# Performance work log

Measured on AMD Instinct MI355X. Metric: run time of the kernel, lower is better.

Reference implementation:

```python
import jax, jax.numpy as jnp
import numpy as np
import math

B, SQ, SK, H, D = 4, 2048, 2048, 16, 128
IS_CAUSAL = True
SCALE = 1.0 / math.sqrt(D)


def setup_inputs() -> dict:
    key = jax.random.key(0)
    kq, kk, kv = jax.random.split(key, 3)
    query = jax.random.normal(kq, (B, SQ, H, D), dtype=jnp.float32)
    key_t = jax.random.normal(kk, (B, SK, H, D), dtype=jnp.float32)
    value = jax.random.normal(kv, (B, SK, H, D), dtype=jnp.float32)
    return {"query": query, "key": key_t, "value": value}


def reference(query, key, value):
    # q: [B, Sq, H, D], k: [B, Sk, H, D], v: [B, Sk, H, Dv]
    scores = jnp.einsum('bqhd,bkhd->bhqk', query, key) * SCALE  # [B, H, Sq, Sk]
    if IS_CAUSAL:
        causal = jnp.triu(jnp.ones((SQ, SK), dtype=jnp.bool_), k=1)  # True above diag
        scores = jnp.where(causal[None, None, :, :], jnp.float32(-jnp.inf), scores)
    attn = jax.nn.softmax(scores, axis=-1)  # stable softmax (== exp(scores - lse))
    out = jnp.einsum('bhqk,bkhd->bqhd', attn, value)  # [B, Sq, H, Dv]
    return out
```

## Files before the change

### kernel.cpp

```cpp
#include <hip/hip_runtime.h>
#include <hip/hip_bf16.h>

typedef float  f32x16 __attribute__((ext_vector_type(16)));
typedef float  f32x4  __attribute__((ext_vector_type(4)));
typedef short  s16x8  __attribute__((ext_vector_type(8)));
typedef unsigned int u32x4 __attribute__((ext_vector_type(4)));

#define B_   4
#define SQ_  2048
#define SK_  2048
#define H_   16
#define D_   128
#define RS   (H_*D_)
#define QSCALE 0.12751219658526f
#define KVB  64
#define QTILE 256
#define KB_BYTES  (64*128*2)
#define BUF_BYTES (2*KB_BYTES)

__device__ __forceinline__ unsigned pk_bf16(float lo, float hi) {
    unsigned r;
    asm("v_cvt_pk_bf16_f32 %0, %1, %2" : "=v"(r) : "v"(lo), "v"(hi));
    return r;
}
__device__ __forceinline__ void swap32u(unsigned &a, unsigned &b) {
    asm("v_permlane32_swap_b32 %0, %1" : "+v"(a), "+v"(b));
}
__device__ __forceinline__ int kaddr(int row, int colb) {
    return row * 256 + (colb ^ ((row & 7) << 4));
}
__device__ __forceinline__ int vaddr(int d, int colb) {
    return d * 128 + (colb ^ ((((d & 7) ^ ((d >> 3) & 7))) << 4));
}

__global__ __launch_bounds__(512, 2)
void fattn_fwd(const float* __restrict__ Qg, const float* __restrict__ Kg,
               const float* __restrict__ Vg, float* __restrict__ Og)
{
    __shared__ __align__(16) char smem[2 * BUF_BYTES];

    const int tid = threadIdx.x;
    const int w   = tid >> 6;
    const int l   = tid & 63;
    const int l31 = l & 31;
    const int hi  = l >> 5;

    const int i    = blockIdx.x;
    const int orig = (i & 7) * 64 + (i >> 3);
    const int bh   = orig >> 3;
    const int j    = orig & 7;
    const int tile = ((bh >> 2) & 1) ? j : 7 - j;
    const int b    = bh >> 4;
    const int h    = bh & 15;

    const int q0 = tile * QTILE;
    const int nt = (q0 + QTILE) / KVB;

    const size_t base = ((size_t)b * SK_ * H_ + h) * D_;
    const float* Kp = Kg + base;
    const float* Vp = Vg + base;
    const float* Qp = Qg + base;
    float*       Op = Og + base;

    const int qrow = q0 + w * 32 + l31;
    const float* qptr = Qp + (size_t)qrow * RS + hi * 8;
    s16x8 qf[8];
#pragma unroll
    for (int sl = 0; sl < 8; ++sl) {
        f32x4 a = *(const f32x4*)(qptr + sl * 16);
        f32x4 c = *(const f32x4*)(qptr + sl * 16 + 4);
        u32x4 u;
        u[0] = pk_bf16(a[0] * QSCALE, a[1] * QSCALE);
        u[1] = pk_bf16(a[2] * QSCALE, a[3] * QSCALE);
        u[2] = pk_bf16(c[0] * QSCALE, c[1] * QSCALE);
        u[3] = pk_bf16(c[2] * QSCALE, c[3] * QSCALE);
        qf[sl] = __builtin_bit_cast(s16x8, u);
    }

    const int krow = tid >> 3;
    const int kc   = (tid & 7) * 16;
    const int vkv  = (tid >> 4) * 2;
    const int vc   = (tid & 15) * 8;
    const float* kgp = Kp + (size_t)krow * RS + kc;
    const float* vgp = Vp + (size_t)vkv * RS + vc;

    f32x16 oacc[4];
#pragma unroll
    for (int d = 0; d < 4; ++d)
#pragma unroll
        for (int r = 0; r < 16; ++r) oacc[d][r] = 0.f;
    float m_run = -1e30f, l_run = 0.f;

    {
        f32x4 kr0 = *(const f32x4*)(kgp + 0);
        f32x4 kr1 = *(const f32x4*)(kgp + 4);
        f32x4 kr2 = *(const f32x4*)(kgp + 8);
        f32x4 kr3 = *(const f32x4*)(kgp + 12);
        f32x4 va0 = *(const f32x4*)(vgp + 0);
        f32x4 va1 = *(const f32x4*)(vgp + 4);
        f32x4 vb0 = *(const f32x4*)(vgp + RS);
        f32x4 vb1 = *(const f32x4*)(vgp + RS + 4);
        char* kb = smem;
        char* vb = smem + KB_BYTES;
        u32x4 u0, u1;
        u0[0] = pk_bf16(kr0[0], kr0[1]); u0[1] = pk_bf16(kr0[2], kr0[3]);
        u0[2] = pk_bf16(kr1[0], kr1[1]); u0[3] = pk_bf16(kr1[2], kr1[3]);
        u1[0] = pk_bf16(kr2[0], kr2[1]); u1[1] = pk_bf16(kr2[2], kr2[3]);
        u1[2] = pk_bf16(kr3[0], kr3[1]); u1[3] = pk_bf16(kr3[2], kr3[3]);
        *(u32x4*)(kb + kaddr(krow, kc * 2))      = u0;
        *(u32x4*)(kb + kaddr(krow, kc * 2 + 16)) = u1;
#pragma unroll
        for (int e = 0; e < 4; ++e) {
            *(unsigned*)(vb + vaddr(vc + e,     vkv * 2)) = pk_bf16(va0[e], vb0[e]);
            *(unsigned*)(vb + vaddr(vc + 4 + e, vkv * 2)) = pk_bf16(va1[e], vb1[e]);
        }
    }
    __syncthreads();

    const int qmaxw = q0 + w * 32 + 31;

    for (int t = 0; t < nt; ++t) {
        const int  nxt = t + 1;
        const bool have_next = nxt < nt;

        f32x4 kr0, kr1, kr2, kr3, va0, va1, vb0, vb1;
        if (have_next) {
            const float* kp2 = kgp + (size_t)nxt * KVB * RS;
            const float* vp2 = vgp + (size_t)nxt * KVB * RS;
            kr0 = *(const f32x4*)(kp2 + 0);
            kr1 = *(const f32x4*)(kp2 + 4);
            kr2 = *(const f32x4*)(kp2 + 8);
            kr3 = *(const f32x4*)(kp2 + 12);
            va0 = *(const f32x4*)(vp2 + 0);
            va1 = *(const f32x4*)(vp2 + 4);
            vb0 = *(const f32x4*)(vp2 + RS);
            vb1 = *(const f32x4*)(vp2 + RS + 4);
        }

        const int kvg = t * KVB;
        if (kvg <= qmaxw) {
            const char* kb = smem + (t & 1) * BUF_BYTES;
            const char* vb = kb + KB_BYTES;

            f32x16 s0, s1;
#pragma unroll
            for (int r = 0; r < 16; ++r) { s0[r] = 0.f; s1[r] = 0.f; }
            __builtin_amdgcn_s_setprio(1);
#pragma unroll
            for (int sl = 0; sl < 8; ++sl) {
                const int colb = 32 * sl + 16 * hi;
                s16x8 ka0 = *(const s16x8*)(kb + kaddr(l31,      colb));
                s16x8 ka1 = *(const s16x8*)(kb + kaddr(32 + l31, colb));
                s0 = __builtin_amdgcn_mfma_f32_32x32x16_bf16(ka0, qf[sl], s0, 0, 0, 0);
                s1 = __builtin_amdgcn_mfma_f32_32x32x16_bf16(ka1, qf[sl], s1, 0, 0, 0);
            }
            __builtin_amdgcn_s_setprio(0);

            float pm0 = -1e30f, pm1 = -1e30f, pm2 = -1e30f, pm3 = -1e30f;
#pragma unroll
            for (int r = 0; r < 16; ++r) {
                const int crow = (r & 3) + 8 * (r >> 2) + 4 * hi;
                const int kva  = kvg + crow;
                if (kva      > qrow) s0[r] = -1e30f;
                if (kva + 32 > qrow) s1[r] = -1e30f;
                const float mr = fmaxf(s0[r], s1[r]);
                if ((r & 3) == 0) pm0 = fmaxf(pm0, mr);
                if ((r & 3) == 1) pm1 = fmaxf(pm1, mr);
                if ((r & 3) == 2) pm2 = fmaxf(pm2, mr);
                if ((r & 3) == 3) pm3 = fmaxf(pm3, mr);
            }
            float pmax = fmaxf(fmaxf(pm0, pm1), fmaxf(pm2, pm3));
            pmax = fmaxf(pmax, __shfl_xor(pmax, 32));

            if (__any(pmax > m_run + 8.0f)) {
                const float mnew = fmaxf(m_run, pmax);
                const float f = exp2f(m_run - mnew);
                m_run = mnew;
                l_run *= f;
#pragma unroll
                for (int d = 0; d < 4; ++d)
#pragma unroll
                    for (int r = 0; r < 16; ++r) oacc[d][r] *= f;
            }

            float ps0 = 0.f, ps1 = 0.f, ps2 = 0.f, ps3 = 0.f;
#pragma unroll
            for (int r = 0; r < 16; ++r) {
                s0[r] = exp2f(s0[r] - m_run);
                s1[r] = exp2f(s1[r] - m_run);
                const float sr = s0[r] + s1[r];
                if ((r & 3) == 0) ps0 += sr;
                if ((r & 3) == 1) ps1 += sr;
                if ((r & 3) == 2) ps2 += sr;
                if ((r & 3) == 3) ps3 += sr;
            }
            float psum = (ps0 + ps1) + (ps2 + ps3);
            psum += __shfl_xor(psum, 32);
            l_run += psum;

            s16x8 pb[4];
            {
                unsigned w00 = pk_bf16(s0[0],  s0[1]);
                unsigned w01 = pk_bf16(s0[2],  s0[3]);
                unsigned w10 = pk_bf16(s0[4],  s0[5]);
                unsigned w11 = pk_bf16(s0[6],  s0[7]);
                unsigned w20 = pk_bf16(s0[8],  s0[9]);
                unsigned w21 = pk_bf16(s0[10], s0[11]);
                unsigned w30 = pk_bf16(s0[12], s0[13]);
                unsigned w31 = pk_bf16(s0[14], s0[15]);
                swap32u(w00, w10); swap32u(w01, w11);
                swap32u(w20, w30); swap32u(w21, w31);
                u32x4 p0; p0[0] = w00; p0[1] = w01; p0[2] = w10; p0[3] = w11;
                u32x4 p1; p1[0] = w20; p1[1] = w21; p1[2] = w30; p1[3] = w31;
                pb[0] = __builtin_bit_cast(s16x8, p0);
                pb[1] = __builtin_bit_cast(s16x8, p1);
                unsigned x00 = pk_bf16(s1[0],  s1[1]);
                unsigned x01 = pk_bf16(s1[2],  s1[3]);
                unsigned x10 = pk_bf16(s1[4],  s1[5]);
                unsigned x11 = pk_bf16(s1[6],  s1[7]);
                unsigned x20 = pk_bf16(s1[8],  s1[9]);
                unsigned x21 = pk_bf16(s1[10], s1[11]);
                unsigned x30 = pk_bf16(s1[12], s1[13]);
                unsigned x31 = pk_bf16(s1[14], s1[15]);
                swap32u(x00, x10); swap32u(x01, x11);
                swap32u(x20, x30); swap32u(x21, x31);
                u32x4 p2; p2[0] = x00; p2[1] = x01; p2[2] = x10; p2[3] = x11;
                u32x4 p3; p3[0] = x20; p3[1] = x21; p3[2] = x30; p3[3] = x31;
                pb[2] = __builtin_bit_cast(s16x8, p2);
                pb[3] = __builtin_bit_cast(s16x8, p3);
            }

            __builtin_amdgcn_s_setprio(1);
#pragma unroll
            for (int db = 0; db < 4; ++db) {
                const int d = 32 * db + l31;
#pragma unroll
                for (int ks = 0; ks < 4; ++ks) {
                    s16x8 va = *(const s16x8*)(vb + vaddr(d, 32 * ks + 16 * hi));
                    oacc[db] = __builtin_amdgcn_mfma_f32_32x32x16_bf16(va, pb[ks], oacc[db], 0, 0, 0);
                }
            }
            __builtin_amdgcn_s_setprio(0);
        }

        __syncthreads();
        if (have_next) {
            char* kb = smem + (nxt & 1) * BUF_BYTES;
            char* vb = kb + KB_BYTES;
            u32x4 u0, u1;
            u0[0] = pk_bf16(kr0[0], kr0[1]); u0[1] = pk_bf16(kr0[2], kr0[3]);
            u0[2] = pk_bf16(kr1[0], kr1[1]); u0[3] = pk_bf16(kr1[2], kr1[3]);
            u1[0] = pk_bf16(kr2[0], kr2[1]); u1[1] = pk_bf16(kr2[2], kr2[3]);
            u1[2] = pk_bf16(kr3[0], kr3[1]); u1[3] = pk_bf16(kr3[2], kr3[3]);
            *(u32x4*)(kb + kaddr(krow, kc * 2))      = u0;
            *(u32x4*)(kb + kaddr(krow, kc * 2 + 16)) = u1;
#pragma unroll
            for (int e = 0; e < 4; ++e) {
                *(unsigned*)(vb + vaddr(vc + e,     vkv * 2)) = pk_bf16(va0[e], vb0[e]);
                *(unsigned*)(vb + vaddr(vc + 4 + e, vkv * 2)) = pk_bf16(va1[e], vb1[e]);
            }
        }
        __syncthreads();
    }

    const float inv = 1.0f / l_run;
    float* op = Op + (size_t)qrow * RS;
#pragma unroll
    for (int db = 0; db < 4; ++db)
#pragma unroll
        for (int rq = 0; rq < 4; ++rq) {
            f32x4 o4;
            o4[0] = oacc[db][4 * rq + 0] * inv;
            o4[1] = oacc[db][4 * rq + 1] * inv;
            o4[2] = oacc[db][4 * rq + 2] * inv;
            o4[3] = oacc[db][4 * rq + 3] * inv;
            *(f32x4*)(op + 32 * db + 8 * rq + 4 * hi) = o4;
        }
}

extern "C" void kernel_launch(void* const* d_in, const int* in_sizes, int n_in,
                              void* d_out, int out_size, void* d_ws, size_t ws_size,
                              hipStream_t stream) {
    const float* Q = (const float*)d_in[0];
    const float* K = (const float*)d_in[1];
    const float* V = (const float*)d_in[2];
    float* O = (float*)d_out;
    (void)in_sizes; (void)n_in; (void)out_size; (void)d_ws; (void)ws_size;
    dim3 grid(B_ * H_ * (SQ_ / QTILE));
    dim3 block(512);
    hipLaunchKernelGGL(fattn_fwd, grid, block, 0, stream, Q, K, V, O);
}
```

Measured before the change: 361.1 us.

## Switch to 16x16x32 MFMA with 128-row query tiles and four blocks per CU

```diff
diff --git a/kernel.cpp b/kernel.cpp
--- a/kernel.cpp
+++ b/kernel.cpp
@@ -1,7 +1,6 @@
 #include <hip/hip_runtime.h>
 #include <hip/hip_bf16.h>
 
-typedef float  f32x16 __attribute__((ext_vector_type(16)));
 typedef float  f32x4  __attribute__((ext_vector_type(4)));
 typedef short  s16x8  __attribute__((ext_vector_type(8)));
 typedef unsigned int u32x4 __attribute__((ext_vector_type(4)));
@@ -13,9 +12,10 @@
 #define D_   128
 #define RS   (H_*D_)
 #define QSCALE 0.12751219658526f
-#define KVB  64
-#define QTILE 256
-#define KB_BYTES  (64*128*2)
+#define KVB   64
+#define QTILE 128
+#define NQT   (SQ_/QTILE)
+#define KB_BYTES  (KVB*D_*2)
 #define BUF_BYTES (2*KB_BYTES)
 
 __device__ __forceinline__ unsigned pk_bf16(float lo, float hi) {
@@ -33,7 +33,7 @@
     return d * 128 + (colb ^ ((((d & 7) ^ ((d >> 3) & 7))) << 4));
 }
 
-__global__ __launch_bounds__(512, 2)
+__global__ __launch_bounds__(512, 4)
 void fattn_fwd(const float* __restrict__ Qg, const float* __restrict__ Kg,
                const float* __restrict__ Vg, float* __restrict__ Og)
 {
@@ -42,53 +42,69 @@
     const int tid = threadIdx.x;
     const int w   = tid >> 6;
     const int l   = tid & 63;
-    const int l31 = l & 31;
-    const int hi  = l >> 5;
-
-    const int i    = blockIdx.x;
-    const int orig = (i & 7) * 64 + (i >> 3);
-    const int bh   = orig >> 3;
-    const int j    = orig & 7;
-    const int tile = ((bh >> 2) & 1) ? j : 7 - j;
-    const int b    = bh >> 4;
-    const int h    = bh & 15;
-
-    const int q0 = tile * QTILE;
-    const int nt = (q0 + QTILE) / KVB;
+    const int g   = l >> 4;
+    const int q   = l & 15;
+
+    const int r   = blockIdx.x;
+    const int qt  = (NQT - 1) - (r >> 6);
+    const int i6  = r & 63;
+    const int bh  = (i6 & 7) * 8 + (i6 >> 3);
+    const int b   = bh >> 4;
+    const int h   = bh & 15;
+    const int q0  = qt * QTILE;
+    const int nt  = 2 * (qt + 1);
 
     const size_t base = ((size_t)b * SK_ * H_ + h) * D_;
+    const float* Qp = Qg + base;
     const float* Kp = Kg + base;
     const float* Vp = Vg + base;
-    const float* Qp = Qg + base;
     float*       Op = Og + base;
 
-    const int qrow = q0 + w * 32 + l31;
-    const float* qptr = Qp + (size_t)qrow * RS + hi * 8;
-    s16x8 qf[8];
-#pragma unroll
-    for (int sl = 0; sl < 8; ++sl) {
-        f32x4 a = *(const f32x4*)(qptr + sl * 16);
-        f32x4 c = *(const f32x4*)(qptr + sl * 16 + 4);
+    const int qrow = q0 + w * 16 + q;
+    const float* qptr = Qp + (size_t)qrow * RS;
+    s16x8 qf[4];
+#pragma unroll
+    for (int kt = 0; kt < 4; ++kt) {
+        const float* p = qptr + 32 * kt + 8 * g;
+        f32x4 a = *(const f32x4*)(p);
+        f32x4 c = *(const f32x4*)(p + 4);
         u32x4 u;
         u[0] = pk_bf16(a[0] * QSCALE, a[1] * QSCALE);
         u[1] = pk_bf16(a[2] * QSCALE, a[3] * QSCALE);
         u[2] = pk_bf16(c[0] * QSCALE, c[1] * QSCALE);
         u[3] = pk_bf16(c[2] * QSCALE, c[3] * QSCALE);
-        qf[sl] = __builtin_bit_cast(s16x8, u);
+        qf[kt] = __builtin_bit_cast(s16x8, u);
     }
 
     const int krow = tid >> 3;
     const int kc   = (tid & 7) * 16;
     const int vkv  = (tid >> 4) * 2;
     const int vc   = (tid & 15) * 8;
+    const int ckv  = (vkv & ~12) | ((vkv & 4) << 1) | ((vkv & 8) >> 1);
     const float* kgp = Kp + (size_t)krow * RS + kc;
     const float* vgp = Vp + (size_t)vkv * RS + vc;
 
-    f32x16 oacc[4];
-#pragma unroll
-    for (int d = 0; d < 4; ++d)
-#pragma unroll
-        for (int r = 0; r < 16; ++r) oacc[d][r] = 0.f;
+    auto stage = [&](char* dst, f32x4 kr0, f32x4 kr1, f32x4 kr2, f32x4 kr3,
+                     f32x4 va0, f32x4 va1, f32x4 vb0, f32x4 vb1) {
+        char* kb = dst;
+        char* vb = dst + KB_BYTES;
+        u32x4 u0, u1;
+        u0[0] = pk_bf16(kr0[0], kr0[1]); u0[1] = pk_bf16(kr0[2], kr0[3]);
+        u0[2] = pk_bf16(kr1[0], kr1[1]); u0[3] = pk_bf16(kr1[2], kr1[3]);
+        u1[0] = pk_bf16(kr2[0], kr2[1]); u1[1] = pk_bf16(kr2[2], kr2[3]);
+        u1[2] = pk_bf16(kr3[0], kr3[1]); u1[3] = pk_bf16(kr3[2], kr3[3]);
+        *(u32x4*)(kb + kaddr(krow, kc * 2))      = u0;
+        *(u32x4*)(kb + kaddr(krow, kc * 2 + 16)) = u1;
+#pragma unroll
+        for (int e = 0; e < 4; ++e) {
+            *(unsigned*)(vb + vaddr(vc + e,     ckv * 2)) = pk_bf16(va0[e], vb0[e]);
+            *(unsigned*)(vb + vaddr(vc + 4 + e, ckv * 2)) = pk_bf16(va1[e], vb1[e]);
+        }
+    };
+
+    f32x4 oacc[8];
+#pragma unroll
+    for (int i = 0; i < 8; ++i) { oacc[i][0] = 0.f; oacc[i][1] = 0.f; oacc[i][2] = 0.f; oacc[i][3] = 0.f; }
     float m_run = -1e30f, l_run = 0.f;
 
     {
@@ -100,24 +116,12 @@
         f32x4 va1 = *(const f32x4*)(vgp + 4);
         f32x4 vb0 = *(const f32x4*)(vgp + RS);
         f32x4 vb1 = *(const f32x4*)(vgp + RS + 4);
-        char* kb = smem;
-        char* vb = smem + KB_BYTES;
-        u32x4 u0, u1;
-        u0[0] = pk_bf16(kr0[0], kr0[1]); u0[1] = pk_bf16(kr0[2], kr0[3]);
-        u0[2] = pk_bf16(kr1[0], kr1[1]); u0[3] = pk_bf16(kr1[2], kr1[3]);
-        u1[0] = pk_bf16(kr2[0], kr2[1]); u1[1] = pk_bf16(kr2[2], kr2[3]);
-        u1[2] = pk_bf16(kr3[0], kr3[1]); u1[3] = pk_bf16(kr3[2], kr3[3]);
-        *(u32x4*)(kb + kaddr(krow, kc * 2))      = u0;
-        *(u32x4*)(kb + kaddr(krow, kc * 2 + 16)) = u1;
-#pragma unroll
-        for (int e = 0; e < 4; ++e) {
-            *(unsigned*)(vb + vaddr(vc + e,     vkv * 2)) = pk_bf16(va0[e], vb0[e]);
-            *(unsigned*)(vb + vaddr(vc + 4 + e, vkv * 2)) = pk_bf16(va1[e], vb1[e]);
-        }
+        stage(smem, kr0, kr1, kr2, kr3, va0, va1, vb0, vb1);
     }
     __syncthreads();
 
-    const int qmaxw = q0 + w * 32 + 31;
+    const int qminw = q0 + w * 16;
+    const int qmaxw = qminw + 15;
 
     for (int t = 0; t < nt; ++t) {
         const int  nxt = t + 1;
@@ -142,34 +146,37 @@
             const char* kb = smem + (t & 1) * BUF_BYTES;
             const char* vb = kb + KB_BYTES;
 
-            f32x16 s0, s1;
-#pragma unroll
-            for (int r = 0; r < 16; ++r) { s0[r] = 0.f; s1[r] = 0.f; }
+            f32x4 s[4];
+#pragma unroll
+            for (int kvs = 0; kvs < 4; ++kvs) { s[kvs][0]=0.f; s[kvs][1]=0.f; s[kvs][2]=0.f; s[kvs][3]=0.f; }
             __builtin_amdgcn_s_setprio(1);
 #pragma unroll
-            for (int sl = 0; sl < 8; ++sl) {
-                const int colb = 32 * sl + 16 * hi;
-                s16x8 ka0 = *(const s16x8*)(kb + kaddr(l31,      colb));
-                s16x8 ka1 = *(const s16x8*)(kb + kaddr(32 + l31, colb));
-                s0 = __builtin_amdgcn_mfma_f32_32x32x16_bf16(ka0, qf[sl], s0, 0, 0, 0);
-                s1 = __builtin_amdgcn_mfma_f32_32x32x16_bf16(ka1, qf[sl], s1, 0, 0, 0);
+            for (int kt = 0; kt < 4; ++kt) {
+                const int colb = 64 * kt + 16 * g;
+#pragma unroll
+                for (int kvs = 0; kvs < 4; ++kvs) {
+                    s16x8 ka = *(const s16x8*)(kb + kaddr(16 * kvs + q, colb));
+                    s[kvs] = __builtin_amdgcn_mfma_f32_16x16x32_bf16(ka, qf[kt], s[kvs], 0, 0, 0);
+                }
             }
             __builtin_amdgcn_s_setprio(0);
 
-            float pm0 = -1e30f, pm1 = -1e30f, pm2 = -1e30f, pm3 = -1e30f;
-#pragma unroll
-            for (int r = 0; r < 16; ++r) {
-                const int crow = (r & 3) + 8 * (r >> 2) + 4 * hi;
-                const int kva  = kvg + crow;
-                if (kva      > qrow) s0[r] = -1e30f;
-                if (kva + 32 > qrow) s1[r] = -1e30f;
-                const float mr = fmaxf(s0[r], s1[r]);
-                if ((r & 3) == 0) pm0 = fmaxf(pm0, mr);
-                if ((r & 3) == 1) pm1 = fmaxf(pm1, mr);
-                if ((r & 3) == 2) pm2 = fmaxf(pm2, mr);
-                if ((r & 3) == 3) pm3 = fmaxf(pm3, mr);
-            }
-            float pmax = fmaxf(fmaxf(pm0, pm1), fmaxf(pm2, pm3));
+            if (kvg + KVB - 1 > qminw) {
+#pragma unroll
+                for (int kvs = 0; kvs < 4; ++kvs)
+#pragma unroll
+                    for (int rr = 0; rr < 4; ++rr) {
+                        const int kva = kvg + 16 * kvs + 4 * g + rr;
+                        if (kva > qrow) s[kvs][rr] = -1e30f;
+                    }
+            }
+
+            float pmax = -1e30f;
+#pragma unroll
+            for (int kvs = 0; kvs < 4; ++kvs)
+#pragma unroll
+                for (int rr = 0; rr < 4; ++rr) pmax = fmaxf(pmax, s[kvs][rr]);
+            pmax = fmaxf(pmax, __shfl_xor(pmax, 16));
             pmax = fmaxf(pmax, __shfl_xor(pmax, 32));
 
             if (__any(pmax > m_run + 8.0f)) {
@@ -178,66 +185,44 @@
                 m_run = mnew;
                 l_run *= f;
 #pragma unroll
-                for (int d = 0; d < 4; ++d)
-#pragma unroll
-                    for (int r = 0; r < 16; ++r) oacc[d][r] *= f;
-            }
-
-            float ps0 = 0.f, ps1 = 0.f, ps2 = 0.f, ps3 = 0.f;
-#pragma unroll
-            for (int r = 0; r < 16; ++r) {
-                s0[r] = exp2f(s0[r] - m_run);
-                s1[r] = exp2f(s1[r] - m_run);
-                const float sr = s0[r] + s1[r];
-                if ((r & 3) == 0) ps0 += sr;
-                if ((r & 3) == 1) ps1 += sr;
-                if ((r & 3) == 2) ps2 += sr;
-                if ((r & 3) == 3) ps3 += sr;
-            }
-            float psum = (ps0 + ps1) + (ps2 + ps3);
+                for (int i = 0; i < 8; ++i) {
+                    oacc[i][0] *= f; oacc[i][1] *= f; oacc[i][2] *= f; oacc[i][3] *= f;
+                }
+            }
+
+            float psum = 0.f;
+#pragma unroll
+            for (int kvs = 0; kvs < 4; ++kvs)
+#pragma unroll
+                for (int rr = 0; rr < 4; ++rr) {
+                    s[kvs][rr] = exp2f(s[kvs][rr] - m_run);
+                    psum += s[kvs][rr];
+                }
+            psum += __shfl_xor(psum, 16);
             psum += __shfl_xor(psum, 32);
             l_run += psum;
 
-            s16x8 pb[4];
-            {
-                unsigned w00 = pk_bf16(s0[0],  s0[1]);
-                unsigned w01 = pk_bf16(s0[2],  s0[3]);
-                unsigned w10 = pk_bf16(s0[4],  s0[5]);
-                unsigned w11 = pk_bf16(s0[6],  s0[7]);
-                unsigned w20 = pk_bf16(s0[8],  s0[9]);
-                unsigned w21 = pk_bf16(s0[10], s0[11]);
-                unsigned w30 = pk_bf16(s0[12], s0[13]);
-                unsigned w31 = pk_bf16(s0[14], s0[15]);
-                swap32u(w00, w10); swap32u(w01, w11);
-                swap32u(w20, w30); swap32u(w21, w31);
-                u32x4 p0; p0[0] = w00; p0[1] = w01; p0[2] = w10; p0[3] = w11;
-                u32x4 p1; p1[0] = w20; p1[1] = w21; p1[2] = w30; p1[3] = w31;
-                pb[0] = __builtin_bit_cast(s16x8, p0);
-                pb[1] = __builtin_bit_cast(s16x8, p1);
-                unsigned x00 = pk_bf16(s1[0],  s1[1]);
-                unsigned x01 = pk_bf16(s1[2],  s1[3]);
-                unsigned x10 = pk_bf16(s1[4],  s1[5]);
-                unsigned x11 = pk_bf16(s1[6],  s1[7]);
-                unsigned x20 = pk_bf16(s1[8],  s1[9]);
-                unsigned x21 = pk_bf16(s1[10], s1[11]);
-                unsigned x30 = pk_bf16(s1[12], s1[13]);
-                unsigned x31 = pk_bf16(s1[14], s1[15]);
-                swap32u(x00, x10); swap32u(x01, x11);
-                swap32u(x20, x30); swap32u(x21, x31);
-                u32x4 p2; p2[0] = x00; p2[1] = x01; p2[2] = x10; p2[3] = x11;
-                u32x4 p3; p3[0] = x20; p3[1] = x21; p3[2] = x30; p3[3] = x31;
-                pb[2] = __builtin_bit_cast(s16x8, p2);
-                pb[3] = __builtin_bit_cast(s16x8, p3);
+            s16x8 pb[2];
+#pragma unroll
+            for (int kt2 = 0; kt2 < 2; ++kt2) {
+                unsigned A0 = pk_bf16(s[2 * kt2][0],     s[2 * kt2][1]);
+                unsigned A1 = pk_bf16(s[2 * kt2][2],     s[2 * kt2][3]);
+                unsigned B0 = pk_bf16(s[2 * kt2 + 1][0], s[2 * kt2 + 1][1]);
+                unsigned B1 = pk_bf16(s[2 * kt2 + 1][2], s[2 * kt2 + 1][3]);
+                swap32u(A0, B0);
+                swap32u(A1, B1);
+                u32x4 p; p[0] = A0; p[1] = A1; p[2] = B0; p[3] = B1;
+                pb[kt2] = __builtin_bit_cast(s16x8, p);
             }
 
             __builtin_amdgcn_s_setprio(1);
 #pragma unroll
-            for (int db = 0; db < 4; ++db) {
-                const int d = 32 * db + l31;
-#pragma unroll
-                for (int ks = 0; ks < 4; ++ks) {
-                    s16x8 va = *(const s16x8*)(vb + vaddr(d, 32 * ks + 16 * hi));
-                    oacc[db] = __builtin_amdgcn_mfma_f32_32x32x16_bf16(va, pb[ks], oacc[db], 0, 0, 0);
+            for (int ds = 0; ds < 8; ++ds) {
+                const int d = 16 * ds + q;
+#pragma unroll
+                for (int kt2 = 0; kt2 < 2; ++kt2) {
+                    s16x8 va = *(const s16x8*)(vb + vaddr(d, 64 * kt2 + 16 * g));
+                    oacc[ds] = __builtin_amdgcn_mfma_f32_16x16x32_bf16(va, pb[kt2], oacc[ds], 0, 0, 0);
                 }
             }
             __builtin_amdgcn_s_setprio(0);
@@ -245,20 +230,7 @@
 
         __syncthreads();
         if (have_next) {
-            char* kb = smem + (nxt & 1) * BUF_BYTES;
-            char* vb = kb + KB_BYTES;
-            u32x4 u0, u1;
-            u0[0] = pk_bf16(kr0[0], kr0[1]); u0[1] = pk_bf16(kr0[2], kr0[3]);
-            u0[2] = pk_bf16(kr1[0], kr1[1]); u0[3] = pk_bf16(kr1[2], kr1[3]);
-            u1[0] = pk_bf16(kr2[0], kr2[1]); u1[1] = pk_bf16(kr2[2], kr2[3]);
-            u1[2] = pk_bf16(kr3[0], kr3[1]); u1[3] = pk_bf16(kr3[2], kr3[3]);
-            *(u32x4*)(kb + kaddr(krow, kc * 2))      = u0;
-            *(u32x4*)(kb + kaddr(krow, kc * 2 + 16)) = u1;
-#pragma unroll
-            for (int e = 0; e < 4; ++e) {
-                *(unsigned*)(vb + vaddr(vc + e,     vkv * 2)) = pk_bf16(va0[e], vb0[e]);
-                *(unsigned*)(vb + vaddr(vc + 4 + e, vkv * 2)) = pk_bf16(va1[e], vb1[e]);
-            }
+            stage(smem + (nxt & 1) * BUF_BYTES, kr0, kr1, kr2, kr3, va0, va1, vb0, vb1);
         }
         __syncthreads();
     }
@@ -266,16 +238,14 @@
     const float inv = 1.0f / l_run;
     float* op = Op + (size_t)qrow * RS;
 #pragma unroll
-    for (int db = 0; db < 4; ++db)
-#pragma unroll
-        for (int rq = 0; rq < 4; ++rq) {
-            f32x4 o4;
-            o4[0] = oacc[db][4 * rq + 0] * inv;
-            o4[1] = oacc[db][4 * rq + 1] * inv;
-            o4[2] = oacc[db][4 * rq + 2] * inv;
-            o4[3] = oacc[db][4 * rq + 3] * inv;
-            *(f32x4*)(op + 32 * db + 8 * rq + 4 * hi) = o4;
-        }
+    for (int ds = 0; ds < 8; ++ds) {
+        f32x4 o4;
+        o4[0] = oacc[ds][0] * inv;
+        o4[1] = oacc[ds][1] * inv;
+        o4[2] = oacc[ds][2] * inv;
+        o4[3] = oacc[ds][3] * inv;
+        *(f32x4*)(op + 16 * ds + 4 * g) = o4;
+    }
 }
 
 extern "C" void kernel_launch(void* const* d_in, const int* in_sizes, int n_in,
@@ -286,7 +256,7 @@
     const float* V = (const float*)d_in[2];
     float* O = (float*)d_out;
     (void)in_sizes; (void)n_in; (void)out_size; (void)d_ws; (void)ws_size;
-    dim3 grid(B_ * H_ * (SQ_ / QTILE));
+    dim3 grid(B_ * H_ * NQT);
     dim3 block(512);
     hipLaunchKernelGGL(fattn_fwd, grid, block, 0, stream, Q, K, V, O);
 }
```

Result: slower. 528.4 us (+46.3%).
